# Kernel tuning notes

Hardware: AMD Instinct MI355X
Metric: run time of the kernel (lower is better)

Reference implementation:

```python
import jax, jax.numpy as jnp
import numpy as np

K = 9          # temporal window (kernel_size)
PAD = (K - 1) // 2
BN_EPS = 1e-5


def setup_inputs() -> dict:
    key = jax.random.key(0)
    ks = jax.random.split(key, 9)
    N, Cin, Cout, T, V = 16, 64, 128, 256, 25
    return {
        "x": jax.random.normal(ks[0], (N, Cin, T, V), jnp.float32),
        "conv_w": jax.random.normal(ks[1], (Cout, Cin), jnp.float32) * (1.0 / np.sqrt(Cin)),
        "conv_b": jax.random.normal(ks[2], (Cout,), jnp.float32) * 0.01,
        "gamma": jax.random.uniform(ks[3], (Cout,), jnp.float32, 0.5, 1.5),
        "beta": jax.random.normal(ks[4], (Cout,), jnp.float32) * 0.1,
        "run_mean": jax.random.normal(ks[5], (Cout,), jnp.float32) * 0.1,
        "run_var": jax.random.uniform(ks[6], (Cout,), jnp.float32, 0.5, 1.5),
        "att0": jnp.full((1, Cout, 1, K), 1.0 / K, jnp.float32),
        "A": jax.random.uniform(ks[7], (V, V), jnp.float32),
        "keep_prob": 1,
    }


def reference(x, conv_w, conv_b, gamma, beta, run_mean, run_var, att0, A, keep_prob):
    # 1x1 conv (pointwise channel mix); AvgPool2d((1,1)) is identity for stride=1
    x = jnp.einsum("nctv,oc->notv", x, conv_w) + conv_b[None, :, None, None]
    # BatchNorm2d (eval mode: running stats)
    scale = gamma / jnp.sqrt(run_var + BN_EPS)
    x = x * scale[None, :, None, None] + (beta - run_mean * scale)[None, :, None, None]
    N, C, T, V = x.shape
    # UnfoldTemporalWindows: zero-pad T, gather K temporal shifts -> (N, C, T, K, V)
    xp = jnp.pad(x, ((0, 0), (0, 0), (PAD, PAD), (0, 0)))
    upfold = jnp.stack([xp[:, :, u:u + T, :] for u in range(K)], axis=3)
    # local attention: score each window position against the center frame
    scores = jnp.einsum("nctv,nctuv->nctu", x, upfold) / V
    attn = jax.nn.softmax(scores, axis=-1) + att0
    out = jnp.einsum("nctuv,nctu->nctv", upfold, attn)
    # dropS / dropT are identity at keep_prob == 1 (inference)
    return out
```

## Files before the change

kernel.cpp:

```cpp
#include <hip/hip_runtime.h>
#include <hip/hip_bf16.h>

#define CIN   64
#define COUT  128
#define TT    256
#define VV    25
#define TV    (TT * VV)
#define KW    9
#define PAD   4
#define YROW  28
#define YSTR  (TT * YROW)

typedef __attribute__((ext_vector_type(8))) short short8;
typedef __attribute__((ext_vector_type(4))) float f32x4;

__device__ __forceinline__ unsigned f2b(float f) {
    unsigned u = __builtin_bit_cast(unsigned, f);
    return (u + 0x7FFFu + ((u >> 16) & 1u)) >> 16;
}
__device__ __forceinline__ float lof(unsigned u) {
    return __builtin_bit_cast(float, u << 16);
}
__device__ __forceinline__ float hif(unsigned u) {
    return __builtin_bit_cast(float, u & 0xffff0000u);
}
__device__ __forceinline__ int swz(int row, int cbyte) {
    return row * 128 + ((cbyte & ~15) ^ ((row & 7) << 4)) + (cbyte & 15);
}

__global__ __launch_bounds__(256) void conv_mfma(
    const float* __restrict__ x, const float* __restrict__ w,
    const float* __restrict__ cb, const float* __restrict__ gamma,
    const float* __restrict__ beta, const float* __restrict__ rm,
    const float* __restrict__ rv, unsigned short* __restrict__ y)
{
    __shared__ __align__(16) unsigned short Wl[COUT * 64];
    __shared__ __align__(16) unsigned short Xl[128 * 64];
    __shared__ float sc[COUT];
    __shared__ float of[COUT];

    const int pc  = blockIdx.x;
    const int n   = blockIdx.y;
    const int tid = threadIdx.x;
    const int posbase = pc * 128;

    if (tid < COUT) {
        const float s = gamma[tid] * rsqrtf(rv[tid] + 1e-5f);
        sc[tid] = s;
        of[tid] = cb[tid] * s + beta[tid] - rm[tid] * s;
    }
    for (int idx = tid; idx < 2048; idx += 256) {
        const int c4 = idx & 15, o = idx >> 4;
        const f32x4 wv = *(const f32x4*)(w + o * 64 + c4 * 4);
        uint2 pk;
        pk.x = f2b(wv.x) | (f2b(wv.y) << 16);
        pk.y = f2b(wv.z) | (f2b(wv.w) << 16);
        *(uint2*)((char*)Wl + swz(o, c4 * 8)) = pk;
    }
    for (int idx = tid; idx < 2048; idx += 256) {
        const int pos = idx & 127, c4 = idx >> 7;
        const float* xp = x + (size_t)n * CIN * TV + (size_t)(c4 * 4) * TV + posbase + pos;
        const float a0 = xp[0], a1 = xp[TV], a2 = xp[2 * TV], a3 = xp[3 * TV];
        uint2 pk;
        pk.x = f2b(a0) | (f2b(a1) << 16);
        pk.y = f2b(a2) | (f2b(a3) << 16);
        *(uint2*)((char*)Xl + swz(pos, c4 * 8)) = pk;
    }
    __syncthreads();

    const int wv_ = tid >> 6, lane = tid & 63;
    const int lr = lane & 15, lh = lane >> 4;

    short8 afr[2][2];
#pragma unroll
    for (int m0 = 0; m0 < 2; ++m0)
#pragma unroll
        for (int kh = 0; kh < 2; ++kh)
            afr[m0][kh] = *(const short8*)((const char*)Wl +
                              swz(wv_ * 32 + m0 * 16 + lr, kh * 64 + lh * 16));

    f32x4 acc[2][8];
#pragma unroll
    for (int m0 = 0; m0 < 2; ++m0)
#pragma unroll
        for (int n0 = 0; n0 < 8; ++n0) acc[m0][n0] = (f32x4){0.f, 0.f, 0.f, 0.f};

#pragma unroll
    for (int n0 = 0; n0 < 8; ++n0) {
        const int prow = n0 * 16 + lr;
        const short8 b0 = *(const short8*)((const char*)Xl + swz(prow, lh * 16));
        const short8 b1 = *(const short8*)((const char*)Xl + swz(prow, 64 + lh * 16));
#pragma unroll
        for (int m0 = 0; m0 < 2; ++m0) {
            acc[m0][n0] = __builtin_amdgcn_mfma_f32_16x16x32_bf16(afr[m0][0], b0, acc[m0][n0], 0, 0, 0);
            acc[m0][n0] = __builtin_amdgcn_mfma_f32_16x16x32_bf16(afr[m0][1], b1, acc[m0][n0], 0, 0, 0);
        }
    }

    float scv[2][4], ofv[2][4];
#pragma unroll
    for (int m0 = 0; m0 < 2; ++m0)
#pragma unroll
        for (int r = 0; r < 4; ++r) {
            const int o = wv_ * 32 + m0 * 16 + lh * 4 + r;
            scv[m0][r] = sc[o];
            ofv[m0][r] = of[o];
        }

    const size_t ybase = (size_t)(n * COUT) * YSTR;
#pragma unroll
    for (int m0 = 0; m0 < 2; ++m0)
#pragma unroll
        for (int n0 = 0; n0 < 8; ++n0)
#pragma unroll
            for (int r = 0; r < 4; ++r) {
                const int o = wv_ * 32 + m0 * 16 + lh * 4 + r;
                const int pos = posbase + n0 * 16 + lr;
                const int t = pos / 25;
                const int v = pos - t * 25;
                const float val = acc[m0][n0][r] * scv[m0][r] + ofv[m0][r];
                y[ybase + (size_t)o * YSTR + t * YROW + v] = (unsigned short)f2b(val);
            }
}

#define LOADROW(lr, dst)                                                    \
    {                                                                       \
        const int ub_ = 7 * (lr);                                           \
        const uint2 r0_ = tl2[ub_],     r1_ = tl2[ub_ + 1];                 \
        const uint2 r2_ = tl2[ub_ + 2], r3_ = tl2[ub_ + 3];                 \
        const uint2 r4_ = tl2[ub_ + 4], r5_ = tl2[ub_ + 5];                 \
        const unsigned l_ = tlu[14 * (lr) + 12];                            \
        (dst)[0]  = lof(r0_.x); (dst)[1]  = hif(r0_.x);                     \
        (dst)[2]  = lof(r0_.y); (dst)[3]  = hif(r0_.y);                     \
        (dst)[4]  = lof(r1_.x); (dst)[5]  = hif(r1_.x);                     \
        (dst)[6]  = lof(r1_.y); (dst)[7]  = hif(r1_.y);                     \
        (dst)[8]  = lof(r2_.x); (dst)[9]  = hif(r2_.x);                     \
        (dst)[10] = lof(r2_.y); (dst)[11] = hif(r2_.y);                     \
        (dst)[12] = lof(r3_.x); (dst)[13] = hif(r3_.x);                     \
        (dst)[14] = lof(r3_.y); (dst)[15] = hif(r3_.y);                     \
        (dst)[16] = lof(r4_.x); (dst)[17] = hif(r4_.x);                     \
        (dst)[18] = lof(r4_.y); (dst)[19] = hif(r4_.y);                     \
        (dst)[20] = lof(r5_.x); (dst)[21] = hif(r5_.x);                     \
        (dst)[22] = lof(r5_.y); (dst)[23] = hif(r5_.y);                     \
        (dst)[24] = lof(l_);                                                \
    }

__global__ __launch_bounds__(256) void attn_kernel(
    const unsigned short* __restrict__ y, const float* __restrict__ att0,
    float* __restrict__ out)
{
    __shared__ __align__(16) float sm[TV];
    __shared__ float a0s[KW];

    uint4* tl4 = (uint4*)sm;
    const uint2* tl2 = (const uint2*)sm;
    const unsigned* tlu = (const unsigned*)sm;

    const int nc  = blockIdx.x;
    const int c   = nc & (COUT - 1);
    const int tid = threadIdx.x;

    if (tid < KW) a0s[tid] = att0[c * KW + tid];

    if (tid < 28) {
        const int i = (tid < 14) ? tid : (896 + tid);
        tl4[i] = make_uint4(0, 0, 0, 0);
    }
    const uint4* yg = (const uint4*)(y + (size_t)nc * YSTR);
#pragma unroll
    for (int i = 0; i < 4; ++i) {
        const int ci = tid + i * 256;
        if (ci < 896) tl4[14 + ci] = yg[ci];
    }
    __syncthreads();

    const int t = tid;

    float q[25];
    LOADROW(t + 4, q);

    float osm[25], oa0[25];
    float den;
    {
        float d0 = 0.f, d1 = 0.f;
#pragma unroll
        for (int v = 0; v < 12; ++v)  d0 = fmaf(q[v], q[v], d0);
#pragma unroll
        for (int v = 12; v < 25; ++v) d1 = fmaf(q[v], q[v], d1);
        const float e = __expf((d0 + d1) * (1.f / 25.f));
        den = e;
        const float a = a0s[4];
#pragma unroll
        for (int v = 0; v < 25; ++v) { osm[v] = e * q[v]; oa0[v] = a * q[v]; }
    }

#pragma unroll
    for (int j = 0; j < KW; ++j) {
        if (j == 4) continue;
        float row[25];
        LOADROW(t + j, row);
        float d0 = 0.f, d1 = 0.f;
#pragma unroll
        for (int v = 0; v < 12; ++v)  d0 = fmaf(row[v], q[v], d0);
#pragma unroll
        for (int v = 12; v < 25; ++v) d1 = fmaf(row[v], q[v], d1);
        const float e = __expf((d0 + d1) * (1.f / 25.f));
        den += e;
        const float a = a0s[j];
#pragma unroll
        for (int v = 0; v < 25; ++v) {
            osm[v] = fmaf(e, row[v], osm[v]);
            oa0[v] = fmaf(a, row[v], oa0[v]);
        }
    }

    const float inv = 1.f / den;

    __syncthreads();
    {
        float* dst = &sm[t * 25];
#pragma unroll
        for (int v = 0; v < 25; ++v) dst[v] = fmaf(osm[v], inv, oa0[v]);
    }
    __syncthreads();

    {
        float4* og = (float4*)(out + (size_t)nc * TV);
        const float4* sm4 = (const float4*)sm;
#pragma unroll
        for (int i = 0; i < 7; ++i) {
            const int ci = tid + i * 256;
            if (ci < TV / 4) og[ci] = sm4[ci];
        }
    }
}

extern "C" void kernel_launch(void* const* d_in, const int* in_sizes, int n_in,
                              void* d_out, int out_size, void* d_ws, size_t ws_size,
                              hipStream_t stream)
{
    const float* x     = (const float*)d_in[0];
    const float* w     = (const float*)d_in[1];
    const float* cb    = (const float*)d_in[2];
    const float* gamma = (const float*)d_in[3];
    const float* beta  = (const float*)d_in[4];
    const float* rm    = (const float*)d_in[5];
    const float* rv    = (const float*)d_in[6];
    const float* att0  = (const float*)d_in[7];
    float* out = (float*)d_out;
    unsigned short* y = (unsigned short*)d_ws;

    dim3 gA(TV / 128, 16);
    conv_mfma<<<gA, 256, 0, stream>>>(x, w, cb, gamma, beta, rm, rv, y);

    dim3 gB(16 * COUT);
    attn_kernel<<<gB, 256, 0, stream>>>(y, att0, out);
}
```

Measured before the change: 44.64 us.

## Store conv output densely and swap MFMA operands for packed vector stores

The intermediate bf16 tensor is now written in a dense T*V layout instead of padded 28-wide rows. Swapping the A/B MFMA operands lets each lane hold four consecutive positions, so it can write them as one packed 8-byte store instead of scattered 2-byte stores. The attention kernel then repacks each 25-element row into the padded shared-memory layout with per-thread unaligned 32-bit loads and shifts. This shrinks the intermediate buffer and makes the writes coalesced, at the cost of more complex, less coalesced reads in the second kernel.

```diff
diff --git a/kernel.cpp b/kernel.cpp
--- a/kernel.cpp
+++ b/kernel.cpp
@@ -8,8 +8,6 @@
 #define TV    (TT * VV)
 #define KW    9
 #define PAD   4
-#define YROW  28
-#define YSTR  (TT * YROW)
 
 typedef __attribute__((ext_vector_type(8))) short short8;
 typedef __attribute__((ext_vector_type(4))) float f32x4;
@@ -71,65 +69,55 @@
     const int wv_ = tid >> 6, lane = tid & 63;
     const int lr = lane & 15, lh = lane >> 4;
 
-    short8 afr[2][2];
-#pragma unroll
-    for (int m0 = 0; m0 < 2; ++m0)
+    short8 bw[2][2];
+#pragma unroll
+    for (int nn = 0; nn < 2; ++nn)
 #pragma unroll
         for (int kh = 0; kh < 2; ++kh)
-            afr[m0][kh] = *(const short8*)((const char*)Wl +
-                              swz(wv_ * 32 + m0 * 16 + lr, kh * 64 + lh * 16));
-
-    f32x4 acc[2][8];
-#pragma unroll
-    for (int m0 = 0; m0 < 2; ++m0)
-#pragma unroll
-        for (int n0 = 0; n0 < 8; ++n0) acc[m0][n0] = (f32x4){0.f, 0.f, 0.f, 0.f};
-
-#pragma unroll
-    for (int n0 = 0; n0 < 8; ++n0) {
-        const int prow = n0 * 16 + lr;
-        const short8 b0 = *(const short8*)((const char*)Xl + swz(prow, lh * 16));
-        const short8 b1 = *(const short8*)((const char*)Xl + swz(prow, 64 + lh * 16));
-#pragma unroll
-        for (int m0 = 0; m0 < 2; ++m0) {
-            acc[m0][n0] = __builtin_amdgcn_mfma_f32_16x16x32_bf16(afr[m0][0], b0, acc[m0][n0], 0, 0, 0);
-            acc[m0][n0] = __builtin_amdgcn_mfma_f32_16x16x32_bf16(afr[m0][1], b1, acc[m0][n0], 0, 0, 0);
-        }
-    }
-
-    float scv[2][4], ofv[2][4];
-#pragma unroll
-    for (int m0 = 0; m0 < 2; ++m0)
-#pragma unroll
-        for (int r = 0; r < 4; ++r) {
-            const int o = wv_ * 32 + m0 * 16 + lh * 4 + r;
-            scv[m0][r] = sc[o];
-            ofv[m0][r] = of[o];
-        }
-
-    const size_t ybase = (size_t)(n * COUT) * YSTR;
-#pragma unroll
-    for (int m0 = 0; m0 < 2; ++m0)
-#pragma unroll
-        for (int n0 = 0; n0 < 8; ++n0)
-#pragma unroll
-            for (int r = 0; r < 4; ++r) {
-                const int o = wv_ * 32 + m0 * 16 + lh * 4 + r;
-                const int pos = posbase + n0 * 16 + lr;
-                const int t = pos / 25;
-                const int v = pos - t * 25;
-                const float val = acc[m0][n0][r] * scv[m0][r] + ofv[m0][r];
-                y[ybase + (size_t)o * YSTR + t * YROW + v] = (unsigned short)f2b(val);
-            }
-}
-
-#define LOADROW(lr, dst)                                                    \
+            bw[nn][kh] = *(const short8*)((const char*)Wl +
+                              swz(wv_ * 32 + nn * 16 + lr, kh * 64 + lh * 16));
+
+    f32x4 acc[8][2];
+#pragma unroll
+    for (int m = 0; m < 8; ++m)
+#pragma unroll
+        for (int nn = 0; nn < 2; ++nn) acc[m][nn] = (f32x4){0.f, 0.f, 0.f, 0.f};
+
+#pragma unroll
+    for (int m = 0; m < 8; ++m) {
+        const int prow = m * 16 + lr;
+        const short8 a0 = *(const short8*)((const char*)Xl + swz(prow, lh * 16));
+        const short8 a1 = *(const short8*)((const char*)Xl + swz(prow, 64 + lh * 16));
+#pragma unroll
+        for (int nn = 0; nn < 2; ++nn) {
+            acc[m][nn] = __builtin_amdgcn_mfma_f32_16x16x32_bf16(a0, bw[nn][0], acc[m][nn], 0, 0, 0);
+            acc[m][nn] = __builtin_amdgcn_mfma_f32_16x16x32_bf16(a1, bw[nn][1], acc[m][nn], 0, 0, 0);
+        }
+    }
+
+#pragma unroll
+    for (int nn = 0; nn < 2; ++nn) {
+        const int o = wv_ * 32 + nn * 16 + lr;
+        const float s = sc[o], f = of[o];
+        unsigned short* yb = y + (size_t)(n * COUT + o) * TV + posbase + lh * 4;
+#pragma unroll
+        for (int m = 0; m < 8; ++m) {
+            const f32x4 a = acc[m][nn];
+            uint2 pk;
+            pk.x = f2b(a[0] * s + f) | (f2b(a[1] * s + f) << 16);
+            pk.y = f2b(a[2] * s + f) | (f2b(a[3] * s + f) << 16);
+            *(uint2*)(yb + m * 16) = pk;
+        }
+    }
+}
+
+#define LOADROW(lr_, dst)                                                   \
     {                                                                       \
-        const int ub_ = 7 * (lr);                                           \
+        const int ub_ = 7 * (lr_);                                          \
         const uint2 r0_ = tl2[ub_],     r1_ = tl2[ub_ + 1];                 \
         const uint2 r2_ = tl2[ub_ + 2], r3_ = tl2[ub_ + 3];                 \
         const uint2 r4_ = tl2[ub_ + 4], r5_ = tl2[ub_ + 5];                 \
-        const unsigned l_ = tlu[14 * (lr) + 12];                            \
+        const unsigned l_ = tlu[14 * (lr_) + 12];                           \
         (dst)[0]  = lof(r0_.x); (dst)[1]  = hif(r0_.x);                     \
         (dst)[2]  = lof(r0_.y); (dst)[3]  = hif(r0_.y);                     \
         (dst)[4]  = lof(r1_.x); (dst)[5]  = hif(r1_.x);                     \
@@ -155,6 +143,7 @@
     uint4* tl4 = (uint4*)sm;
     const uint2* tl2 = (const uint2*)sm;
     const unsigned* tlu = (const unsigned*)sm;
+    unsigned* tlw = (unsigned*)sm;
 
     const int nc  = blockIdx.x;
     const int c   = nc & (COUT - 1);
@@ -166,11 +155,21 @@
         const int i = (tid < 14) ? tid : (896 + tid);
         tl4[i] = make_uint4(0, 0, 0, 0);
     }
-    const uint4* yg = (const uint4*)(y + (size_t)nc * YSTR);
-#pragma unroll
-    for (int i = 0; i < 4; ++i) {
-        const int ci = tid + i * 256;
-        if (ci < 896) tl4[14 + ci] = yg[ci];
+
+    {
+        const unsigned* ygu = (const unsigned*)(y + (size_t)nc * TV);
+        const int t = tid;
+        const int s0 = (25 * t) >> 1;
+        const int odd = t & 1;
+        unsigned u[14];
+#pragma unroll
+        for (int i = 0; i < 14; ++i) u[i] = ygu[min(s0 + i, 3199)];
+        unsigned* dst = tlw + 14 * (t + 4);
+#pragma unroll
+        for (int d = 0; d < 13; ++d) {
+            const unsigned shifted = (u[d] >> 16) | (u[d + 1] << 16);
+            dst[d] = odd ? shifted : u[d];
+        }
     }
     __syncthreads();
 
```

Result: no change. 44.54 us, median of 2 (-0.2%).
